# Optimization experiments

Hardware: AMD Instinct MI355X
Metric: run time of the kernel (lower is better)

## Reference

```python
import jax, jax.numpy as jnp
import numpy as np

SHAPES = ((64, 64), (32, 32), (16, 16))   # H/8, H/16, H/32 levels of a 512x512 image
B, D = 32, 256
NH, L, P = 8, 3, 4                        # MSDeformAttn heads / levels / points
DH = D // NH
NCLS, NC, NH_CA = 200, 10, 2
LQ = 32 * 32
LIN = sum(h * w for h, w in SHAPES)


def _ref_points():
    # get_reference_points for the H/16 grid, normalized (x, y) in (0,1)
    H_, W_ = 32, 32
    ry, rx = np.meshgrid(np.linspace(0.5, H_ - 0.5, H_) / H_,
                         np.linspace(0.5, W_ - 0.5, W_) / W_, indexing='ij')
    ref = np.stack([rx.ravel(), ry.ravel()], -1).astype(np.float32)  # (Lq, 2)
    return jnp.asarray(ref)[None, :, None, :]                        # (1, Lq, 1, 2)


def _msda(query, feats, W_off, b_off, W_attn, b_attn, W_val, b_val, W_out, b_out):
    """Multi-scale deformable attention (grid_sample bilinear, align_corners=False, zero pad)."""
    value = (feats @ W_val + b_val).reshape(B, LIN, NH, DH)
    off = (query @ W_off + b_off).reshape(B, LQ, NH, L, P, 2)
    aw = jax.nn.softmax((query @ W_attn + b_attn).reshape(B, LQ, NH, L * P), -1)
    aw = aw.reshape(B, LQ, NH, L, P)
    norm = jnp.asarray([[w, h] for h, w in SHAPES], jnp.float32)     # (L, 2) as (W, H)
    ref = _ref_points()                                              # (1, Lq, 1, 2)
    loc = ref[:, :, None, :, None, :] + off / norm[None, None, None, :, None, :]  # (B,Lq,NH,L,P,2)

    out = jnp.zeros((B, NH, LQ, DH), query.dtype)
    start = 0
    for lvl, (H_, W_) in enumerate(SHAPES):
        v = value[:, start:start + H_ * W_].transpose(0, 2, 1, 3)    # (B, NH, HW, DH)
        start += H_ * W_
        lx = loc[:, :, :, lvl, :, 0] * W_ - 0.5                      # (B, Lq, NH, P)
        ly = loc[:, :, :, lvl, :, 1] * H_ - 0.5
        x0 = jnp.floor(lx).astype(jnp.int32)
        y0 = jnp.floor(ly).astype(jnp.int32)
        dx = (lx - x0).transpose(0, 2, 1, 3)                         # (B, NH, Lq, P)
        dy = (ly - y0).transpose(0, 2, 1, 3)

        def gather(ix, iy):
            valid = (ix >= 0) & (ix < W_) & (iy >= 0) & (iy < H_)
            idx = (jnp.clip(iy, 0, H_ - 1) * W_ + jnp.clip(ix, 0, W_ - 1))
            idx = idx.transpose(0, 2, 1, 3).reshape(B, NH, LQ * P)
            g = jnp.take_along_axis(v, idx[..., None], axis=2).reshape(B, NH, LQ, P, DH)
            return g * valid.transpose(0, 2, 1, 3)[..., None]

        samp = (gather(x0,     y0)     * ((1 - dx) * (1 - dy))[..., None]
              + gather(x0 + 1, y0)     * (dx * (1 - dy))[..., None]
              + gather(x0,     y0 + 1) * ((1 - dx) * dy)[..., None]
              + gather(x0 + 1, y0 + 1) * (dx * dy)[..., None])       # (B,NH,Lq,P,DH)
        out = out + (samp * aw[:, :, :, lvl, :].transpose(0, 2, 1, 3)[..., None]).sum(3)
    out = out.transpose(0, 2, 1, 3).reshape(B, LQ, D)
    return out @ W_out + b_out


def _cross_attn(x, concepts, Wq, bq, Wkv, bkv, Wp, bp):
    Bx, N, _ = x.shape
    M = concepts.shape[1]
    dh = D // NH_CA
    q = (x @ Wq + bq).reshape(Bx, N, NH_CA, dh).transpose(0, 2, 1, 3)          # (B, h, N, dh)
    kv = (concepts @ Wkv + bkv).reshape(1, M, 2, NH_CA, dh).transpose(2, 0, 3, 1, 4)
    k, v = kv[0], kv[1]                                                        # (1, h, M, dh)
    attn = jax.nn.softmax(jnp.einsum('bhnd,ohmd->bhnm', q, k) * (dh ** -0.5), -1)
    o = jnp.einsum('bhnm,ohmd->bhnd', attn, v).transpose(0, 2, 1, 3).reshape(Bx, N, D)
    return o @ Wp + bp, attn


def _forward(query, feats, x_cls, W_off, b_off, W_attn, b_attn, W_val, b_val, W_out, b_out,
             unsup_concepts, concepts, spatial_concepts,
             Wq_c, bq_c, Wkv_c, bkv_c, Wp_c, bp_c,
             Wq_s, bq_s, Wkv_s, bkv_s, Wp_s, bp_s):
    # injector-style residual: query tokens refined by multi-scale deformable attention
    x = query + _msda(query, feats, W_off, b_off, W_attn, b_attn, W_val, b_val, W_out, b_out)
    # NB: original code reuses concept_tranformer for the unsup branch (faithful to source)
    out_u, attn_u = _cross_attn(x_cls, unsup_concepts, Wq_c, bq_c, Wkv_c, bkv_c, Wp_c, bp_c)
    out_n, attn_n = _cross_attn(x_cls, concepts,       Wq_c, bq_c, Wkv_c, bkv_c, Wp_c, bp_c)
    out_s, attn_s = _cross_attn(x,     spatial_concepts, Wq_s, bq_s, Wkv_s, bkv_s, Wp_s, bp_s)
    out = out_u[:, 0] + out_n[:, 0] + out_s.mean(1)                  # (B, num_classes)
    return out, attn_u.mean(1), attn_n.mean(1), attn_s.mean(1)


def setup_inputs() -> dict:
    key = jax.random.key(0)
    ks = jax.random.split(key, 20)
    s = 1.0 / np.sqrt(D)

    def n(i, shape, scale=1.0):
        return jax.random.normal(ks[i], shape, jnp.float32) * scale

    return dict(
        query=n(0, (B, LQ, D)), feats=n(1, (B, LIN, D)), x_cls=n(2, (B, 1, D)),
        W_off=n(3, (D, NH * L * P * 2), 0.01), b_off=n(4, (NH * L * P * 2,), 0.5),
        W_attn=n(5, (D, NH * L * P), 0.01), b_attn=jnp.zeros((NH * L * P,)),
        W_val=n(6, (D, D), s), b_val=jnp.zeros((D,)),
        W_out=n(7, (D, D), s), b_out=jnp.zeros((D,)),
        unsup_concepts=n(8, (1, NC, D), s), concepts=n(9, (1, NC, D), s),
        spatial_concepts=n(10, (1, NC, D), s),
        Wq_c=n(11, (D, D), s), bq_c=jnp.zeros((D,)),
        Wkv_c=n(12, (D, 2 * D), s), bkv_c=jnp.zeros((2 * D,)),
        Wp_c=n(13, (D, NCLS), s), bp_c=jnp.zeros((NCLS,)),
        Wq_s=n(14, (D, D), s), bq_s=jnp.zeros((D,)),
        Wkv_s=n(15, (D, 2 * D), s), bkv_s=jnp.zeros((2 * D,)),
        Wp_s=n(16, (D, NCLS), s), bp_s=jnp.zeros((NCLS,)),
    )


def reference(query, feats, x_cls, W_off, b_off, W_attn, b_attn, W_val, b_val, W_out, b_out,
              unsup_concepts, concepts, spatial_concepts,
              Wq_c, bq_c, Wkv_c, bkv_c, Wp_c, bp_c,
              Wq_s, bq_s, Wkv_s, bkv_s, Wp_s, bp_s):
    return _forward(query, feats, x_cls, W_off, b_off, W_attn, b_attn, W_val, b_val, W_out, b_out,
                    unsup_concepts, concepts, spatial_concepts,
                    Wq_c, bq_c, Wkv_c, bkv_c, Wp_c, bp_c,
                    Wq_s, bq_s, Wkv_s, bkv_s, Wp_s, bp_s)
```

## Files before the change

kernel.cpp:

```cpp
#include <hip/hip_runtime.h>
#include <hip/hip_bf16.h>


typedef __attribute__((ext_vector_type(8))) short s16x8;
typedef __attribute__((ext_vector_type(4))) float f32x4;

__device__ __forceinline__ void store_val(float* p, float v) { *p = v; }
__device__ __forceinline__ void store_val(__hip_bfloat16* p, float v) { *p = __float2bfloat16(v); }

__device__ __forceinline__ unsigned short f2bf(float x) {
  unsigned int u = __builtin_bit_cast(unsigned int, x);
  u += 0x7FFFu + ((u >> 16) & 1u);
  return (unsigned short)(u >> 16);
}
__device__ __forceinline__ float bf2f(unsigned short u) {
  return __builtin_bit_cast(float, (unsigned int)u << 16);
}
__device__ __forceinline__ float bflo(unsigned int u) {
  return __builtin_bit_cast(float, u << 16);
}
__device__ __forceinline__ float bfhi(unsigned int u) {
  return __builtin_bit_cast(float, u & 0xFFFF0000u);
}

__device__ __forceinline__ void gload16(const char* g, char* l) {
  __builtin_amdgcn_global_load_lds(
      (const __attribute__((address_space(1))) unsigned int*)g,
      (__attribute__((address_space(3))) unsigned int*)l, 16, 0, 0);
}

__global__ __launch_bounds__(256) void wt2_kernel(
    const float* __restrict__ W_val, const float* __restrict__ W_off,
    const float* __restrict__ b_off, const float* __restrict__ W_attn,
    const float* __restrict__ b_attn, char* __restrict__ imgV,
    char* __restrict__ imgQ, float* __restrict__ bpack)
{
  const int n = blockIdx.x;
  const int k = threadIdx.x;
  if (n == 576) {
    bpack[k] = (k < 192) ? b_off[k] : ((k < 288) ? b_attn[k - 192] : 0.f);
    if (k < 64) bpack[256 + k] = (k < 32) ? b_attn[64 + k] : 0.f;
    return;
  }
  const int ks = k >> 6;
  const int kb = (k & 63) * 2;
  if (n < 256) {
    const unsigned short v = f2bf(W_val[(size_t)k * 256 + n]);
    *(unsigned short*)(imgV + ks * 32768 + n * 128 + (kb ^ ((n & 7) << 4))) = v;
  } else {
    const int c = n - 256;
    float v = 0.f;
    if (c < 192) v = W_off[(size_t)k * 192 + c];
    else if (c < 288) v = W_attn[(size_t)k * 96 + (c - 192)];
    *(unsigned short*)(imgQ + ks * 40960 + c * 128 + (kb ^ ((c & 7) << 4))) = f2bf(v);
  }
}

template <typename OT, int NCOLS, int MINW>
__global__ __launch_bounds__(512, MINW) void gemm_f32a(
    const float* __restrict__ A, const char* __restrict__ Bimg,
    const float* __restrict__ bias, OT* __restrict__ C)
{
  constexpr int NFR = NCOLS / 64;
  __shared__ char sAf[32768];
  __shared__ char sBb[NCOLS * 128];

  const int tid = threadIdx.x;
  const int lane = tid & 63;
  const int w = tid >> 6;
  const int wr = (w >> 2) * 64;
  const int wc = (w & 3) * (NCOLS / 4);
  const int l15 = lane & 15;
  const int lg = lane >> 4;
  const int m0 = blockIdx.x * 128;

  int asrc[4];
#pragma unroll
  for (int i = 0; i < 4; ++i) {
    const int slot = w * 256 + i * 64 + lane;
    const int row = slot >> 4;
    const int c = (slot & 15) ^ (row & 7);
    asrc[i] = row * 256 + c * 4;
  }
  const float* Abase = A + (size_t)m0 * 256;

  f32x4 acc[4][NFR] = {};

#pragma unroll
  for (int ks = 0; ks < 4; ++ks) {
    if (ks) __syncthreads();
    {
      char* la = sAf + w * 4096;
#pragma unroll
      for (int i = 0; i < 4; ++i)
        gload16((const char*)(Abase + ks * 64 + asrc[i]), la + i * 1024);
      const char* gb = Bimg + ks * (NCOLS * 128) + w * (NCOLS * 16) + lane * 16;
      char* lb = sBb + w * (NCOLS * 16);
#pragma unroll
      for (int i = 0; i < NFR; ++i)
        gload16(gb + i * 1024, lb + i * 1024);
    }
    __syncthreads();
#pragma unroll
    for (int kk = 0; kk < 2; ++kk) {
      const int c0 = kk * 8 + lg * 2;
      s16x8 af[4];
#pragma unroll
      for (int mf = 0; mf < 4; ++mf) {
        const int row = wr + mf * 16 + l15;
        const int sw = row & 7;
        const f32x4 lo = *reinterpret_cast<const f32x4*>(
            sAf + row * 256 + ((c0 ^ sw) * 16));
        const f32x4 hi = *reinterpret_cast<const f32x4*>(
            sAf + row * 256 + (((c0 + 1) ^ sw) * 16));
        uint4 u;
        u.x = (unsigned)f2bf(lo[0]) | ((unsigned)f2bf(lo[1]) << 16);
        u.y = (unsigned)f2bf(lo[2]) | ((unsigned)f2bf(lo[3]) << 16);
        u.z = (unsigned)f2bf(hi[0]) | ((unsigned)f2bf(hi[1]) << 16);
        u.w = (unsigned)f2bf(hi[2]) | ((unsigned)f2bf(hi[3]) << 16);
        af[mf] = __builtin_bit_cast(s16x8, u);
      }
      const int kb = kk * 64 + lg * 16;
      s16x8 bf[NFR];
#pragma unroll
      for (int nf = 0; nf < NFR; ++nf) {
        const int col = wc + nf * 16 + l15;
        bf[nf] = *reinterpret_cast<const s16x8*>(sBb + col * 128 + (kb ^ ((col & 7) << 4)));
      }
#pragma unroll
      for (int mf = 0; mf < 4; ++mf)
#pragma unroll
        for (int nf = 0; nf < NFR; ++nf)
          acc[mf][nf] = __builtin_amdgcn_mfma_f32_16x16x32_bf16(af[mf], bf[nf], acc[mf][nf], 0, 0, 0);
    }
  }

#pragma unroll
  for (int nf = 0; nf < NFR; ++nf) {
    const int col = wc + nf * 16 + l15;
    const float bb = bias[col];
#pragma unroll
    for (int mf = 0; mf < 4; ++mf) {
#pragma unroll
      for (int j = 0; j < 4; ++j) {
        const int row = m0 + wr + mf * 16 + lg * 4 + j;
        store_val(&C[(size_t)row * NCOLS + col], acc[mf][nf][j] + bb);
      }
    }
  }
}

__global__ __launch_bounds__(256) void kv_kernel(
    const float* __restrict__ unsup, const float* __restrict__ conc,
    const float* __restrict__ spat, const float* __restrict__ Wkv_c,
    const float* __restrict__ bkv_c, const float* __restrict__ Wkv_s,
    const float* __restrict__ bkv_s, float* __restrict__ kv_u,
    float* __restrict__ kv_n, float* __restrict__ kv_s)
{
  const int j = blockIdx.x;
  const float* src = (j == 0) ? unsup : ((j == 1) ? conc : spat);
  const float* W   = (j < 2) ? Wkv_c : Wkv_s;
  const float* bb  = (j < 2) ? bkv_c : bkv_s;
  float* dst       = (j == 0) ? kv_u : ((j == 1) ? kv_n : kv_s);
  __shared__ float s[2560];
  for (int i = threadIdx.x; i < 2560; i += 256) s[i] = src[i];
  __syncthreads();
  for (int o = threadIdx.x; o < 5120; o += 256) {
    const int m = o >> 9, n = o & 511;
    float acc = bb[n];
    for (int k = 0; k < 256; ++k) acc += s[m * 256 + k] * W[(size_t)k * 512 + n];
    dst[o] = acc;
  }
}

__global__ __launch_bounds__(256) void prep_kernel(
    const float* __restrict__ Wq_s, const float* __restrict__ bq_s,
    const float* __restrict__ W_out, const float* __restrict__ b_out,
    const float* __restrict__ kv_s, float* __restrict__ WLt,
    float* __restrict__ WL2t, float* __restrict__ cL)
{
  const int j = blockIdx.x;
  const int h = j / 10, m = j % 10;
  const int tid = threadIdx.x;
  __shared__ float kk[128], wl[256], bred[256];
  if (tid < 128) kk[tid] = kv_s[m * 512 + h * 128 + tid];
  __syncthreads();
  float acc = 0.f;
  for (int e = 0; e < 128; ++e) acc += Wq_s[(size_t)tid * 256 + h * 128 + e] * kk[e];
  wl[tid] = acc;
  __syncthreads();
  float acc2 = 0.f;
  for (int t = 0; t < 256; ++t) acc2 += W_out[(size_t)tid * 256 + t] * wl[t];
  const float scale = 0.08838834764831845f;
  WLt[j * 256 + tid] = scale * acc;
  WL2t[j * 256 + tid] = scale * acc2;
  bred[tid] = b_out[tid] * wl[tid] + ((tid < 128) ? bq_s[h * 128 + tid] * kk[tid] : 0.f);
  __syncthreads();
  for (int s = 128; s > 0; s >>= 1) {
    if (tid < s) bred[tid] += bred[tid + s];
    __syncthreads();
  }
  if (tid == 0) cL[j] = scale * bred[0];
}

__global__ __launch_bounds__(256) void msda_kernel8(
    const float* __restrict__ offlog, const __hip_bfloat16* __restrict__ value,
    __hip_bfloat16* __restrict__ msda_out)
{
  const int bq0 = blockIdx.x * 8;
  const int b = bq0 >> 10;
  const int tid = threadIdx.x;
  __shared__ float aw[768];
  __shared__ int4 sRow[768];
  __shared__ float4 sW[768];

  if (tid < 64) {
    const int qi = tid >> 3, h = tid & 7;
    const float* lp = &offlog[(size_t)(bq0 + qi) * 320 + 192 + h * 12];
    float e[12];
    float mx = -1e30f;
#pragma unroll
    for (int i = 0; i < 12; ++i) { e[i] = lp[i]; mx = fmaxf(mx, e[i]); }
    float s = 0.f;
#pragma unroll
    for (int i = 0; i < 12; ++i) { e[i] = expf(e[i] - mx); s += e[i]; }
    const float inv = 1.f / s;
#pragma unroll
    for (int i = 0; i < 12; ++i) aw[qi * 96 + h * 12 + i] = e[i] * inv;
  }
  __syncthreads();

#pragma unroll
  for (int k = 0; k < 3; ++k) {
    const int j = k * 256 + tid;
    const int qi = j / 96, cc = j - qi * 96;
    const int q = (bq0 + qi) & 1023;
    const int h = cc / 12, r = cc - h * 12, l = r >> 2, p_ = r & 3;
    const int WHl[3] = {64, 32, 16};
    const int St[3] = {0, 4096, 5120};
    const float2 o2 = *reinterpret_cast<const float2*>(
        &offlog[(size_t)(bq0 + qi) * 320 + h * 24 + l * 8 + p_ * 2]);
    const float refx = ((q & 31) + 0.5f) * (1.0f / 32.0f);
    const float refy = ((q >> 5) + 0.5f) * (1.0f / 32.0f);
    const int WH = WHl[l];
    const float fw = (float)WH;
    const float lx = (refx + o2.x / fw) * fw - 0.5f;
    const float ly = (refy + o2.y / fw) * fw - 0.5f;
    const float fx = floorf(lx), fy = floorf(ly);
    const int x0 = (int)fx, y0 = (int)fy;
    const float dx = lx - fx, dy = ly - fy;
    const float a = aw[j];
    int rows[4];
    float ws[4];
#pragma unroll
    for (int c = 0; c < 4; ++c) {
      const int ix = x0 + (c & 1), iy = y0 + (c >> 1);
      const float wb = ((c & 1) ? dx : 1.f - dx) * ((c >> 1) ? dy : 1.f - dy);
      const bool valid = (ix >= 0) && (ix < WH) && (iy >= 0) && (iy < WH);
      const int cx = min(max(ix, 0), WH - 1);
      const int cy = min(max(iy, 0), WH - 1);
      rows[c] = St[l] + cy * WH + cx;
      ws[c] = valid ? wb * a : 0.f;
    }
    sRow[j] = int4{rows[0], rows[1], rows[2], rows[3]};
    sW[j] = float4{ws[0], ws[1], ws[2], ws[3]};
  }
  __syncthreads();

  const int qi = tid >> 5;
  const int h = (tid >> 2) & 7;
  const int d4 = tid & 3;
  const unsigned short* vb = (const unsigned short*)value
      + (size_t)b * (5376 * 256) + h * 32 + d4 * 8;
  const int cbase = qi * 96 + h * 12;
  float acc[8] = {};
#pragma unroll 4
  for (int s = 0; s < 12; ++s) {
    const int4 rows = sRow[cbase + s];
    const float4 wv = sW[cbase + s];
    const int ra[4] = {rows.x, rows.y, rows.z, rows.w};
    const float wa[4] = {wv.x, wv.y, wv.z, wv.w};
#pragma unroll
    for (int c = 0; c < 4; ++c) {
      const uint4 v = *reinterpret_cast<const uint4*>(vb + (size_t)ra[c] * 256);
      const float w = wa[c];
      acc[0] += w * bflo(v.x); acc[1] += w * bfhi(v.x);
      acc[2] += w * bflo(v.y); acc[3] += w * bfhi(v.y);
      acc[4] += w * bflo(v.z); acc[5] += w * bfhi(v.z);
      acc[6] += w * bflo(v.w); acc[7] += w * bfhi(v.w);
    }
  }
  uint4 o;
  o.x = (unsigned)f2bf(acc[0]) | ((unsigned)f2bf(acc[1]) << 16);
  o.y = (unsigned)f2bf(acc[2]) | ((unsigned)f2bf(acc[3]) << 16);
  o.z = (unsigned)f2bf(acc[4]) | ((unsigned)f2bf(acc[5]) << 16);
  o.w = (unsigned)f2bf(acc[6]) | ((unsigned)f2bf(acc[7]) << 16);
  *reinterpret_cast<uint4*>(
      (unsigned short*)msda_out + (size_t)(bq0 + qi) * 256 + h * 32 + d4 * 8) = o;
}

__global__ __launch_bounds__(256) void spatial_kernel(
    const float* __restrict__ query, const __hip_bfloat16* __restrict__ msda,
    const float* __restrict__ WLt, const float* __restrict__ WL2t,
    const float* __restrict__ cL, float* __restrict__ attn_out,
    float* __restrict__ partial)
{
  __shared__ float wls[20][256];
  __shared__ float wl2s[20][256];
  __shared__ float red[128][20];
  const int tid = threadIdx.x;
  for (int i = tid; i < 5120; i += 256) {
    wls[i >> 8][i & 255] = WLt[i];
    wl2s[i >> 8][i & 255] = WL2t[i];
  }
  const int row_local = tid >> 1;
  const int half = tid & 1;
  const int row = blockIdx.x * 128 + row_local;
  float acc[20];
#pragma unroll
  for (int c = 0; c < 20; ++c) acc[c] = half ? 0.f : cL[c];
  __syncthreads();

  const float* qp = &query[(size_t)row * 256 + half * 128];
  const unsigned short* mp = (const unsigned short*)msda + (size_t)row * 256 + half * 128;
  const int kbase = half * 128;
  for (int k = 0; k < 128; k += 4) {
    const f32x4 q4 = *reinterpret_cast<const f32x4*>(qp + k);
    const uint2 mm = *reinterpret_cast<const uint2*>(mp + k);
    const float m0 = bf2f((unsigned short)mm.x);
    const float m1 = bf2f((unsigned short)(mm.x >> 16));
    const float m2 = bf2f((unsigned short)mm.y);
    const float m3 = bf2f((unsigned short)(mm.y >> 16));
#pragma unroll
    for (int c = 0; c < 20; ++c) {
      const f32x4 w4 = *reinterpret_cast<const f32x4*>(&wls[c][kbase + k]);
      const f32x4 v4 = *reinterpret_cast<const f32x4*>(&wl2s[c][kbase + k]);
      acc[c] += q4.x * w4.x + q4.y * w4.y + q4.z * w4.z + q4.w * w4.w
              + m0 * v4.x + m1 * v4.y + m2 * v4.z + m3 * v4.w;
    }
  }
  if (half == 1) {
#pragma unroll
    for (int c = 0; c < 20; ++c) red[row_local][c] = acc[c];
  }
  __syncthreads();
  if (half == 0) {
    float a[20];
#pragma unroll
    for (int c = 0; c < 20; ++c) a[c] = acc[c] + red[row_local][c];
#pragma unroll
    for (int h = 0; h < 2; ++h) {
      float mx = -1e30f;
#pragma unroll
      for (int m = 0; m < 10; ++m) mx = fmaxf(mx, a[h * 10 + m]);
      float s = 0.f;
#pragma unroll
      for (int m = 0; m < 10; ++m) { a[h * 10 + m] = expf(a[h * 10 + m] - mx); s += a[h * 10 + m]; }
      const float inv = 1.f / s;
#pragma unroll
      for (int m = 0; m < 10; ++m) a[h * 10 + m] *= inv;
    }
#pragma unroll
    for (int m = 0; m < 10; ++m)
      attn_out[(size_t)row * 10 + m] = 0.5f * (a[m] + a[10 + m]);
#pragma unroll
    for (int c = 0; c < 20; ++c) red[row_local][c] = a[c];
  }
  __syncthreads();
  if (tid < 20) {
    float s = 0.f;
    for (int r = 0; r < 128; ++r) s += red[r][tid];
    partial[blockIdx.x * 20 + tid] = s;
  }
}

__global__ __launch_bounds__(64) void cls_attn_kernel(
    const float* __restrict__ x_cls, const float* __restrict__ Wq_c,
    const float* __restrict__ bq_c, const float* __restrict__ kv_u,
    const float* __restrict__ kv_n, float* __restrict__ o_un,
    float* __restrict__ attn_u_out, float* __restrict__ attn_n_out)
{
  const int b = blockIdx.x;
  const int lane = threadIdx.x;
  __shared__ float xr[256];
  *reinterpret_cast<float4*>(&xr[lane * 4]) =
      *reinterpret_cast<const float4*>(&x_cls[(size_t)b * 256 + lane * 4]);
  __syncthreads();
  float4 q4 = *reinterpret_cast<const float4*>(&bq_c[lane * 4]);
  for (int k = 0; k < 256; ++k) {
    const float xk = xr[k];
    const float4 w = *reinterpret_cast<const float4*>(&Wq_c[(size_t)k * 256 + lane * 4]);
    q4.x += xk * w.x; q4.y += xk * w.y; q4.z += xk * w.z; q4.w += xk * w.w;
  }
  const float scale = 0.08838834764831845f;
  float4 osum = {0.f, 0.f, 0.f, 0.f};
  for (int cs = 0; cs < 2; ++cs) {
    const float* kv = cs ? kv_n : kv_u;
    float* aout = cs ? attn_n_out : attn_u_out;
    float attn[10];
    float mx = -1e30f;
#pragma unroll
    for (int m = 0; m < 10; ++m) {
      const float4 k4 = *reinterpret_cast<const float4*>(&kv[m * 512 + lane * 4]);
      float p = q4.x * k4.x + q4.y * k4.y + q4.z * k4.z + q4.w * k4.w;
      p += __shfl_xor(p, 1);  p += __shfl_xor(p, 2);  p += __shfl_xor(p, 4);
      p += __shfl_xor(p, 8);  p += __shfl_xor(p, 16);
      attn[m] = p * scale;
      mx = fmaxf(mx, attn[m]);
    }
    float s = 0.f;
#pragma unroll
    for (int m = 0; m < 10; ++m) { attn[m] = expf(attn[m] - mx); s += attn[m]; }
    const float inv = 1.f / s;
#pragma unroll
    for (int m = 0; m < 10; ++m) {
      attn[m] *= inv;
      const float am = 0.5f * (attn[m] + __shfl_xor(attn[m], 32));
      if (lane == m) aout[b * 10 + m] = am;
      const float4 v4 = *reinterpret_cast<const float4*>(&kv[m * 512 + 256 + lane * 4]);
      osum.x += attn[m] * v4.x; osum.y += attn[m] * v4.y;
      osum.z += attn[m] * v4.z; osum.w += attn[m] * v4.w;
    }
  }
  *reinterpret_cast<float4*>(&o_un[(size_t)b * 256 + lane * 4]) = osum;
}

__global__ __launch_bounds__(256) void final_out_kernel(
    const float* __restrict__ o_un, const float* __restrict__ partial,
    const float* __restrict__ kv_s, const float* __restrict__ Wp_c,
    const float* __restrict__ bp_c, const float* __restrict__ Wp_s,
    const float* __restrict__ bp_s, float* __restrict__ out)
{
  const int b = blockIdx.x, c = threadIdx.x;
  __shared__ float ou[256], os[256], abar[20];
  if (c < 20) {
    float s = 0.f;
    for (int ch = 0; ch < 8; ++ch) s += partial[(b * 8 + ch) * 20 + c];
    abar[c] = s * (1.0f / 1024.0f);
  }
  ou[c] = o_un[(size_t)b * 256 + c];
  __syncthreads();
  const int h = c >> 7, d = c & 127;
  float s = 0.f;
#pragma unroll
  for (int m = 0; m < 10; ++m) s += abar[h * 10 + m] * kv_s[m * 512 + 256 + h * 128 + d];
  os[c] = s;
  __syncthreads();
  if (c < 200) {
    float acc = 2.f * bp_c[c] + bp_s[c];
    for (int dd = 0; dd < 256; ++dd)
      acc += ou[dd] * Wp_c[dd * 200 + c] + os[dd] * Wp_s[dd * 200 + c];
    out[b * 200 + c] = acc;
  }
}

extern "C" void kernel_launch(void* const* d_in, const int* in_sizes, int n_in,
                              void* d_out, int out_size, void* d_ws, size_t ws_size,
                              hipStream_t stream)
{
  const float* query  = (const float*)d_in[0];
  const float* feats  = (const float*)d_in[1];
  const float* x_cls  = (const float*)d_in[2];
  const float* W_off  = (const float*)d_in[3];
  const float* b_off  = (const float*)d_in[4];
  const float* W_attn = (const float*)d_in[5];
  const float* b_attn = (const float*)d_in[6];
  const float* W_val  = (const float*)d_in[7];
  const float* b_val  = (const float*)d_in[8];
  const float* W_out  = (const float*)d_in[9];
  const float* b_out  = (const float*)d_in[10];
  const float* unsup  = (const float*)d_in[11];
  const float* conc   = (const float*)d_in[12];
  const float* spat   = (const float*)d_in[13];
  const float* Wq_c   = (const float*)d_in[14];
  const float* bq_c   = (const float*)d_in[15];
  const float* Wkv_c  = (const float*)d_in[16];
  const float* bkv_c  = (const float*)d_in[17];
  const float* Wp_c   = (const float*)d_in[18];
  const float* bp_c   = (const float*)d_in[19];
  const float* Wq_s   = (const float*)d_in[20];
  const float* bq_s   = (const float*)d_in[21];
  const float* Wkv_s  = (const float*)d_in[22];
  const float* bkv_s  = (const float*)d_in[23];
  const float* Wp_s   = (const float*)d_in[24];
  const float* bp_s   = (const float*)d_in[25];
  float* out = (float*)d_out;

  const int B = 32, LQ = 1024, LIN = 5376;
  const int MQ = B * LQ;
  const int MV = B * LIN;

  char* p = (char*)d_ws;
  __hip_bfloat16* value = (__hip_bfloat16*)p;   p += (size_t)MV * 256 * 2;
  float* offlog   = (float*)p;                  p += (size_t)MQ * 320 * 4;
  __hip_bfloat16* msda = (__hip_bfloat16*)p;    p += (size_t)MQ * 256 * 2;
  char* imgV      = p;                          p += 4 * 32768;
  char* imgQ      = p;                          p += 4 * 40960;
  float* bpack    = (float*)p;                  p += 320 * 4;
  float* kv_u     = (float*)p;                  p += 5120 * 4;
  float* kv_n     = (float*)p;                  p += 5120 * 4;
  float* kv_s     = (float*)p;                  p += 5120 * 4;
  float* WLt      = (float*)p;                  p += 5120 * 4;
  float* WL2t     = (float*)p;                  p += 5120 * 4;
  float* cL       = (float*)p;                  p += 32 * 4;
  float* o_un     = (float*)p;                  p += (size_t)B * 256 * 4;
  float* partial  = (float*)p;                  p += 256 * 20 * 4;

  dim3 blk(256);
  wt2_kernel<<<dim3(577), blk, 0, stream>>>(W_val, W_off, b_off, W_attn, b_attn,
                                            imgV, imgQ, bpack);
  kv_kernel<<<dim3(3), blk, 0, stream>>>(unsup, conc, spat, Wkv_c, bkv_c,
                                         Wkv_s, bkv_s, kv_u, kv_n, kv_s);
  prep_kernel<<<dim3(20), blk, 0, stream>>>(Wq_s, bq_s, W_out, b_out, kv_s, WLt, WL2t, cL);
  gemm_f32a<__hip_bfloat16, 256, 4><<<dim3(MV / 128), dim3(512), 0, stream>>>(
      feats, imgV, b_val, value);
  gemm_f32a<float, 320, 2><<<dim3(MQ / 128), dim3(512), 0, stream>>>(
      query, imgQ, bpack, offlog);
  msda_kernel8<<<dim3(MQ / 8), blk, 0, stream>>>(offlog, value, msda);
  spatial_kernel<<<dim3(MQ / 128), blk, 0, stream>>>(
      query, msda, WLt, WL2t, cL, out + 7040, partial);
  cls_attn_kernel<<<dim3(B), dim3(64), 0, stream>>>(
      x_cls, Wq_c, bq_c, kv_u, kv_n, o_un, out + 6400, out + 6720);
  final_out_kernel<<<dim3(B), blk, 0, stream>>>(
      o_un, partial, kv_s, Wp_c, bp_c, Wp_s, bp_s, out);
}
```

Measured before the change: 353.4 us.

## Fuse prep and final kernels; prefetch MSDA value gathers via async LDS loads

Merges the weight-packing, kv projection and spatial prep kernels into one launch, recomputing the needed kv_s slice locally, and merges the class-attention and final output kernels. The MSDA gather loop now issues global-to-LDS async loads for the sampling points two steps ahead into a triple buffer, waiting with explicit vmcnt counts. This aims to hide gather latency and cut launch overhead. In exchange it uses a large LDS buffer that can reduce occupancy, and prep blocks redo some kv work.

```diff
diff --git a/kernel.cpp b/kernel.cpp
--- a/kernel.cpp
+++ b/kernel.cpp
@@ -29,30 +29,87 @@
       (__attribute__((address_space(3))) unsigned int*)l, 16, 0, 0);
 }
 
-__global__ __launch_bounds__(256) void wt2_kernel(
+__global__ __launch_bounds__(256) void prep_all(
     const float* __restrict__ W_val, const float* __restrict__ W_off,
     const float* __restrict__ b_off, const float* __restrict__ W_attn,
     const float* __restrict__ b_attn, char* __restrict__ imgV,
-    char* __restrict__ imgQ, float* __restrict__ bpack)
+    char* __restrict__ imgQ, float* __restrict__ bpack,
+    const float* __restrict__ unsup, const float* __restrict__ conc,
+    const float* __restrict__ spat, const float* __restrict__ Wkv_c,
+    const float* __restrict__ bkv_c, const float* __restrict__ Wkv_s,
+    const float* __restrict__ bkv_s, float* __restrict__ kv_u,
+    float* __restrict__ kv_n, float* __restrict__ kv_s,
+    const float* __restrict__ Wq_s, const float* __restrict__ bq_s,
+    const float* __restrict__ W_out, const float* __restrict__ b_out,
+    float* __restrict__ WLt, float* __restrict__ WL2t, float* __restrict__ cL)
 {
-  const int n = blockIdx.x;
-  const int k = threadIdx.x;
-  if (n == 576) {
-    bpack[k] = (k < 192) ? b_off[k] : ((k < 288) ? b_attn[k - 192] : 0.f);
-    if (k < 64) bpack[256 + k] = (k < 32) ? b_attn[64 + k] : 0.f;
+  const int bi = blockIdx.x;
+  const int tid = threadIdx.x;
+  if (bi <= 576) {
+    const int n = bi, k = tid;
+    if (n == 576) {
+      bpack[k] = (k < 192) ? b_off[k] : ((k < 288) ? b_attn[k - 192] : 0.f);
+      if (k < 64) bpack[256 + k] = (k < 32) ? b_attn[64 + k] : 0.f;
+      return;
+    }
+    const int ks = k >> 6;
+    const int kb = (k & 63) * 2;
+    if (n < 256) {
+      const unsigned short v = f2bf(W_val[(size_t)k * 256 + n]);
+      *(unsigned short*)(imgV + ks * 32768 + n * 128 + (kb ^ ((n & 7) << 4))) = v;
+    } else {
+      const int c = n - 256;
+      float v = 0.f;
+      if (c < 192) v = W_off[(size_t)k * 192 + c];
+      else if (c < 288) v = W_attn[(size_t)k * 96 + (c - 192)];
+      *(unsigned short*)(imgQ + ks * 40960 + c * 128 + (kb ^ ((c & 7) << 4))) = f2bf(v);
+    }
     return;
   }
-  const int ks = k >> 6;
-  const int kb = (k & 63) * 2;
-  if (n < 256) {
-    const unsigned short v = f2bf(W_val[(size_t)k * 256 + n]);
-    *(unsigned short*)(imgV + ks * 32768 + n * 128 + (kb ^ ((n & 7) << 4))) = v;
-  } else {
-    const int c = n - 256;
-    float v = 0.f;
-    if (c < 192) v = W_off[(size_t)k * 192 + c];
-    else if (c < 288) v = W_attn[(size_t)k * 96 + (c - 192)];
-    *(unsigned short*)(imgQ + ks * 40960 + c * 128 + (kb ^ ((c & 7) << 4))) = f2bf(v);
+  if (bi <= 579) {
+    const int j = bi - 577;
+    const float* src = (j == 0) ? unsup : ((j == 1) ? conc : spat);
+    const float* W   = (j < 2) ? Wkv_c : Wkv_s;
+    const float* bb  = (j < 2) ? bkv_c : bkv_s;
+    float* dst       = (j == 0) ? kv_u : ((j == 1) ? kv_n : kv_s);
+    __shared__ float s[2560];
+    for (int i = tid; i < 2560; i += 256) s[i] = src[i];
+    __syncthreads();
+    for (int o = tid; o < 5120; o += 256) {
+      const int m = o >> 9, n = o & 511;
+      float acc = bb[n];
+      for (int k = 0; k < 256; ++k) acc += s[m * 256 + k] * W[(size_t)k * 512 + n];
+      dst[o] = acc;
+    }
+    return;
+  }
+  {
+    const int j = bi - 580;
+    const int h = j / 10, m = j % 10;
+    __shared__ float kk[128], wl[256], bred[256];
+    if (tid < 128) {
+      const int n = h * 128 + tid;
+      float acc = bkv_s[n];
+      for (int k = 0; k < 256; ++k) acc += spat[m * 256 + k] * Wkv_s[(size_t)k * 512 + n];
+      kk[tid] = acc;
+    }
+    __syncthreads();
+    float acc = 0.f;
+    for (int e = 0; e < 128; ++e) acc += Wq_s[(size_t)tid * 256 + h * 128 + e] * kk[e];
+    wl[tid] = acc;
+    __syncthreads();
+    float acc2 = 0.f;
+    for (int t = 0; t < 256; ++t) acc2 += W_out[(size_t)tid * 256 + t] * wl[t];
+    const float scale = 0.08838834764831845f;
+    WLt[j * 256 + tid] = scale * acc;
+    WL2t[j * 256 + tid] = scale * acc2;
+    bred[tid] = b_out[tid] * wl[tid] + ((tid < 128) ? bq_s[h * 128 + tid] * kk[tid] : 0.f);
+    __syncthreads();
+    for (int s = 128; s > 0; s >>= 1) {
+      if (tid < s) bred[tid] += bred[tid + s];
+      __syncthreads();
+    }
+    if (tid == 0) cL[j] = scale * bred[0];
   }
 }
 
@@ -150,60 +207,7 @@
   }
 }
 
-__global__ __launch_bounds__(256) void kv_kernel(
-    const float* __restrict__ unsup, const float* __restrict__ conc,
-    const float* __restrict__ spat, const float* __restrict__ Wkv_c,
-    const float* __restrict__ bkv_c, const float* __restrict__ Wkv_s,
-    const float* __restrict__ bkv_s, float* __restrict__ kv_u,
-    float* __restrict__ kv_n, float* __restrict__ kv_s)
-{
-  const int j = blockIdx.x;
-  const float* src = (j == 0) ? unsup : ((j == 1) ? conc : spat);
-  const float* W   = (j < 2) ? Wkv_c : Wkv_s;
-  const float* bb  = (j < 2) ? bkv_c : bkv_s;
-  float* dst       = (j == 0) ? kv_u : ((j == 1) ? kv_n : kv_s);
-  __shared__ float s[2560];
-  for (int i = threadIdx.x; i < 2560; i += 256) s[i] = src[i];
-  __syncthreads();
-  for (int o = threadIdx.x; o < 5120; o += 256) {
-    const int m = o >> 9, n = o & 511;
-    float acc = bb[n];
-    for (int k = 0; k < 256; ++k) acc += s[m * 256 + k] * W[(size_t)k * 512 + n];
-    dst[o] = acc;
-  }
-}
-
-__global__ __launch_bounds__(256) void prep_kernel(
-    const float* __restrict__ Wq_s, const float* __restrict__ bq_s,
-    const float* __restrict__ W_out, const float* __restrict__ b_out,
-    const float* __restrict__ kv_s, float* __restrict__ WLt,
-    float* __restrict__ WL2t, float* __restrict__ cL)
-{
-  const int j = blockIdx.x;
-  const int h = j / 10, m = j % 10;
-  const int tid = threadIdx.x;
-  __shared__ float kk[128], wl[256], bred[256];
-  if (tid < 128) kk[tid] = kv_s[m * 512 + h * 128 + tid];
-  __syncthreads();
-  float acc = 0.f;
-  for (int e = 0; e < 128; ++e) acc += Wq_s[(size_t)tid * 256 + h * 128 + e] * kk[e];
-  wl[tid] = acc;
-  __syncthreads();
-  float acc2 = 0.f;
-  for (int t = 0; t < 256; ++t) acc2 += W_out[(size_t)tid * 256 + t] * wl[t];
-  const float scale = 0.08838834764831845f;
-  WLt[j * 256 + tid] = scale * acc;
-  WL2t[j * 256 + tid] = scale * acc2;
-  bred[tid] = b_out[tid] * wl[tid] + ((tid < 128) ? bq_s[h * 128 + tid] * kk[tid] : 0.f);
-  __syncthreads();
-  for (int s = 128; s > 0; s >>= 1) {
-    if (tid < s) bred[tid] += bred[tid + s];
-    __syncthreads();
-  }
-  if (tid == 0) cL[j] = scale * bred[0];
-}
-
-__global__ __launch_bounds__(256) void msda_kernel8(
+__global__ __launch_bounds__(256) void msda_v4(
     const float* __restrict__ offlog, const __hip_bfloat16* __restrict__ value,
     __hip_bfloat16* __restrict__ msda_out)
 {
@@ -213,6 +217,7 @@
   __shared__ float aw[768];
   __shared__ int4 sRow[768];
   __shared__ float4 sW[768];
+  __shared__ __align__(16) char gbuf[4 * 3 * 4096];
 
   if (tid < 64) {
     const int qi = tid >> 3, h = tid & 7;
@@ -267,27 +272,51 @@
   }
   __syncthreads();
 
+  const int w = tid >> 6;
+  const int lane = tid & 63;
   const int qi = tid >> 5;
   const int h = (tid >> 2) & 7;
   const int d4 = tid & 3;
   const unsigned short* vb = (const unsigned short*)value
       + (size_t)b * (5376 * 256) + h * 32 + d4 * 8;
   const int cbase = qi * 96 + h * 12;
+  char* gb = gbuf + w * 12288;
+
+#pragma unroll
+  for (int s0 = 0; s0 < 2; ++s0) {
+    const int4 rows = sRow[cbase + s0];
+    const int ra[4] = {rows.x, rows.y, rows.z, rows.w};
+#pragma unroll
+    for (int c = 0; c < 4; ++c)
+      gload16((const char*)(vb + (size_t)ra[c] * 256), gb + s0 * 4096 + c * 1024);
+  }
+
   float acc[8] = {};
-#pragma unroll 4
+#pragma unroll
   for (int s = 0; s < 12; ++s) {
-    const int4 rows = sRow[cbase + s];
+    if (s + 2 < 12) {
+      const int4 rows = sRow[cbase + s + 2];
+      const int ra[4] = {rows.x, rows.y, rows.z, rows.w};
+      const int slot = (s + 2) % 3;
+#pragma unroll
+      for (int c = 0; c < 4; ++c)
+        gload16((const char*)(vb + (size_t)ra[c] * 256), gb + slot * 4096 + c * 1024);
+    }
+    if (s <= 9)       asm volatile("s_waitcnt vmcnt(8)" ::: "memory");
+    else if (s == 10) asm volatile("s_waitcnt vmcnt(4)" ::: "memory");
+    else              asm volatile("s_waitcnt vmcnt(0)" ::: "memory");
+    __builtin_amdgcn_sched_barrier(0);
     const float4 wv = sW[cbase + s];
-    const int ra[4] = {rows.x, rows.y, rows.z, rows.w};
     const float wa[4] = {wv.x, wv.y, wv.z, wv.w};
+    const int slot = s % 3;
 #pragma unroll
     for (int c = 0; c < 4; ++c) {
-      const uint4 v = *reinterpret_cast<const uint4*>(vb + (size_t)ra[c] * 256);
-      const float w = wa[c];
-      acc[0] += w * bflo(v.x); acc[1] += w * bfhi(v.x);
-      acc[2] += w * bflo(v.y); acc[3] += w * bfhi(v.y);
-      acc[4] += w * bflo(v.z); acc[5] += w * bfhi(v.z);
-      acc[6] += w * bflo(v.w); acc[7] += w * bfhi(v.w);
+      const uint4 v = *reinterpret_cast<const uint4*>(gb + slot * 4096 + c * 1024 + lane * 16);
+      const float wgt = wa[c];
+      acc[0] += wgt * bflo(v.x); acc[1] += wgt * bfhi(v.x);
+      acc[2] += wgt * bflo(v.y); acc[3] += wgt * bfhi(v.y);
+      acc[4] += wgt * bflo(v.z); acc[5] += wgt * bfhi(v.z);
+      acc[6] += wgt * bflo(v.w); acc[7] += wgt * bfhi(v.w);
     }
   }
   uint4 o;
@@ -374,83 +403,80 @@
   }
 }
 
-__global__ __launch_bounds__(64) void cls_attn_kernel(
+__global__ __launch_bounds__(256) void final2_kernel(
     const float* __restrict__ x_cls, const float* __restrict__ Wq_c,
     const float* __restrict__ bq_c, const float* __restrict__ kv_u,
-    const float* __restrict__ kv_n, float* __restrict__ o_un,
+    const float* __restrict__ kv_n, const float* __restrict__ partial,
+    const float* __restrict__ kv_s, const float* __restrict__ Wp_c,
+    const float* __restrict__ bp_c, const float* __restrict__ Wp_s,
+    const float* __restrict__ bp_s, float* __restrict__ out,
     float* __restrict__ attn_u_out, float* __restrict__ attn_n_out)
 {
-  const int b = blockIdx.x;
-  const int lane = threadIdx.x;
-  __shared__ float xr[256];
-  *reinterpret_cast<float4*>(&xr[lane * 4]) =
-      *reinterpret_cast<const float4*>(&x_cls[(size_t)b * 256 + lane * 4]);
-  __syncthreads();
-  float4 q4 = *reinterpret_cast<const float4*>(&bq_c[lane * 4]);
-  for (int k = 0; k < 256; ++k) {
-    const float xk = xr[k];
-    const float4 w = *reinterpret_cast<const float4*>(&Wq_c[(size_t)k * 256 + lane * 4]);
-    q4.x += xk * w.x; q4.y += xk * w.y; q4.z += xk * w.z; q4.w += xk * w.w;
-  }
-  const float scale = 0.08838834764831845f;
-  float4 osum = {0.f, 0.f, 0.f, 0.f};
-  for (int cs = 0; cs < 2; ++cs) {
-    const float* kv = cs ? kv_n : kv_u;
-    float* aout = cs ? attn_n_out : attn_u_out;
-    float attn[10];
-    float mx = -1e30f;
-#pragma unroll
-    for (int m = 0; m < 10; ++m) {
-      const float4 k4 = *reinterpret_cast<const float4*>(&kv[m * 512 + lane * 4]);
-      float p = q4.x * k4.x + q4.y * k4.y + q4.z * k4.z + q4.w * k4.w;
-      p += __shfl_xor(p, 1);  p += __shfl_xor(p, 2);  p += __shfl_xor(p, 4);
-      p += __shfl_xor(p, 8);  p += __shfl_xor(p, 16);
-      attn[m] = p * scale;
-      mx = fmaxf(mx, attn[m]);
-    }
-    float s = 0.f;
-#pragma unroll
-    for (int m = 0; m < 10; ++m) { attn[m] = expf(attn[m] - mx); s += attn[m]; }
-    const float inv = 1.f / s;
-#pragma unroll
-    for (int m = 0; m < 10; ++m) {
-      attn[m] *= inv;
-      const float am = 0.5f * (attn[m] + __shfl_xor(attn[m], 32));
-      if (lane == m) aout[b * 10 + m] = am;
-      const float4 v4 = *reinterpret_cast<const float4*>(&kv[m * 512 + 256 + lane * 4]);
-      osum.x += attn[m] * v4.x; osum.y += attn[m] * v4.y;
-      osum.z += attn[m] * v4.z; osum.w += attn[m] * v4.w;
-    }
-  }
-  *reinterpret_cast<float4*>(&o_un[(size_t)b * 256 + lane * 4]) = osum;
-}
-
-__global__ __launch_bounds__(256) void final_out_kernel(
-    const float* __restrict__ o_un, const float* __restrict__ partial,
-    const float* __restrict__ kv_s, const float* __restrict__ Wp_c,
-    const float* __restrict__ bp_c, const float* __restrict__ Wp_s,
-    const float* __restrict__ bp_s, float* __restrict__ out)
-{
-  const int b = blockIdx.x, c = threadIdx.x;
-  __shared__ float ou[256], os[256], abar[20];
-  if (c < 20) {
+  const int b = blockIdx.x, tid = threadIdx.x;
+  __shared__ float ou[256], osb[256], abar[20], xr[256];
+  if (tid < 64)
+    *reinterpret_cast<float4*>(&xr[tid * 4]) =
+        *reinterpret_cast<const float4*>(&x_cls[(size_t)b * 256 + tid * 4]);
+  if (tid >= 64 && tid < 84) {
+    const int c = tid - 64;
     float s = 0.f;
     for (int ch = 0; ch < 8; ++ch) s += partial[(b * 8 + ch) * 20 + c];
     abar[c] = s * (1.0f / 1024.0f);
   }
-  ou[c] = o_un[(size_t)b * 256 + c];
-  __syncthreads();
-  const int h = c >> 7, d = c & 127;
-  float s = 0.f;
-#pragma unroll
-  for (int m = 0; m < 10; ++m) s += abar[h * 10 + m] * kv_s[m * 512 + 256 + h * 128 + d];
-  os[c] = s;
-  __syncthreads();
-  if (c < 200) {
-    float acc = 2.f * bp_c[c] + bp_s[c];
+  __syncthreads();
+  if (tid < 64) {
+    const int lane = tid;
+    float4 q4 = *reinterpret_cast<const float4*>(&bq_c[lane * 4]);
+    for (int k = 0; k < 256; ++k) {
+      const float xk = xr[k];
+      const float4 w = *reinterpret_cast<const float4*>(&Wq_c[(size_t)k * 256 + lane * 4]);
+      q4.x += xk * w.x; q4.y += xk * w.y; q4.z += xk * w.z; q4.w += xk * w.w;
+    }
+    const float scale = 0.08838834764831845f;
+    float4 osum = {0.f, 0.f, 0.f, 0.f};
+    for (int cs = 0; cs < 2; ++cs) {
+      const float* kv = cs ? kv_n : kv_u;
+      float* aout = cs ? attn_n_out : attn_u_out;
+      float attn[10];
+      float mx = -1e30f;
+#pragma unroll
+      for (int m = 0; m < 10; ++m) {
+        const float4 k4 = *reinterpret_cast<const float4*>(&kv[m * 512 + lane * 4]);
+        float p = q4.x * k4.x + q4.y * k4.y + q4.z * k4.z + q4.w * k4.w;
+        p += __shfl_xor(p, 1);  p += __shfl_xor(p, 2);  p += __shfl_xor(p, 4);
+        p += __shfl_xor(p, 8);  p += __shfl_xor(p, 16);
+        attn[m] = p * scale;
+        mx = fmaxf(mx, attn[m]);
+      }
+      float s = 0.f;
+#pragma unroll
+      for (int m = 0; m < 10; ++m) { attn[m] = expf(attn[m] - mx); s += attn[m]; }
+      const float inv = 1.f / s;
+#pragma unroll
+      for (int m = 0; m < 10; ++m) {
+        attn[m] *= inv;
+        const float am = 0.5f * (attn[m] + __shfl_xor(attn[m], 32));
+        if (lane == m) aout[b * 10 + m] = am;
+        const float4 v4 = *reinterpret_cast<const float4*>(&kv[m * 512 + 256 + lane * 4]);
+        osum.x += attn[m] * v4.x; osum.y += attn[m] * v4.y;
+        osum.z += attn[m] * v4.z; osum.w += attn[m] * v4.w;
+      }
+    }
+    *reinterpret_cast<float4*>(&ou[lane * 4]) = osum;
+  }
+  {
+    const int h = tid >> 7, d = tid & 127;
+    float s = 0.f;
+#pragma unroll
+    for (int m = 0; m < 10; ++m) s += abar[h * 10 + m] * kv_s[m * 512 + 256 + h * 128 + d];
+    osb[tid] = s;
+  }
+  __syncthreads();
+  if (tid < 200) {
+    float acc = 2.f * bp_c[tid] + bp_s[tid];
     for (int dd = 0; dd < 256; ++dd)
-      acc += ou[dd] * Wp_c[dd * 200 + c] + os[dd] * Wp_s[dd * 200 + c];
-    out[b * 200 + c] = acc;
+      acc += ou[dd] * Wp_c[dd * 200 + tid] + osb[dd] * Wp_s[dd * 200 + tid];
+    out[b * 200 + tid] = acc;
   }
 }
 
@@ -503,24 +529,21 @@
   float* WLt      = (float*)p;                  p += 5120 * 4;
   float* WL2t     = (float*)p;                  p += 5120 * 4;
   float* cL       = (float*)p;                  p += 32 * 4;
-  float* o_un     = (float*)p;                  p += (size_t)B * 256 * 4;
   float* partial  = (float*)p;                  p += 256 * 20 * 4;
 
   dim3 blk(256);
-  wt2_kernel<<<dim3(577), blk, 0, stream>>>(W_val, W_off, b_off, W_attn, b_attn,
-                                            imgV, imgQ, bpack);
-  kv_kernel<<<dim3(3), blk, 0, stream>>>(unsup, conc, spat, Wkv_c, bkv_c,
-                                         Wkv_s, bkv_s, kv_u, kv_n, kv_s);
-  prep_kernel<<<dim3(20), blk, 0, stream>>>(Wq_s, bq_s, W_out, b_out, kv_s, WLt, WL2t, cL);
+  prep_all<<<dim3(600), blk, 0, stream>>>(
+      W_val, W_off, b_off, W_attn, b_attn, imgV, imgQ, bpack,
+      unsup, conc, spat, Wkv_c, bkv_c, Wkv_s, bkv_s, kv_u, kv_n, kv_s,
+      Wq_s, bq_s, W_out, b_out, WLt, WL2t, cL);
   gemm_f32a<__hip_bfloat16, 256, 4><<<dim3(MV / 128), dim3(512), 0, stream>>>(
       feats, imgV, b_val, value);
   gemm_f32a<float, 320, 2><<<dim3(MQ / 128), dim3(512), 0, stream>>>(
       query, imgQ, bpack, offlog);
-  msda_kernel8<<<dim3(MQ / 8), blk, 0, stream>>>(offlog, value, msda);
+  msda_v4<<<dim3(MQ / 8), blk, 0, stream>>>(offlog, value, msda);
   spatial_kernel<<<dim3(MQ / 128), blk, 0, stream>>>(
       query, msda, WLt, WL2t, cL, out + 7040, partial);
-  cls_attn_kernel<<<dim3(B), dim3(64), 0, stream>>>(
-      x_cls, Wq_c, bq_c, kv_u, kv_n, o_un, out + 6400, out + 6720);
-  final_out_kernel<<<dim3(B), blk, 0, stream>>>(
-      o_un, partial, kv_s, Wp_c, bp_c, Wp_s, bp_s, out);
-}
+  final2_kernel<<<dim3(B), blk, 0, stream>>>(
+      x_cls, Wq_c, bq_c, kv_u, kv_n, partial, kv_s, Wp_c, bp_c, Wp_s, bp_s,
+      out, out + 6400, out + 6720);
+}
```

Result: faster. 320.3 us (-9.4%).
